# Kernel tuning notes

Hardware: AMD Instinct MI355X
Metric: run time of the kernel (lower is better)

Reference implementation:

```python
import jax, jax.numpy as jnp
import numpy as np

GRID_SIZE = 3
SPLINE_ORDER = 3
GRID_RANGE = (-1.0, 1.0)


def make_grid():
    # extended knot vector, shape (1, grid_size + 2*spline_order + 1) = (1, 10)
    h = (GRID_RANGE[1] - GRID_RANGE[0]) / GRID_SIZE
    pts = np.arange(-SPLINE_ORDER, GRID_SIZE + SPLINE_ORDER + 1, dtype=np.float32) * h + GRID_RANGE[0]
    return jnp.asarray(pts[None, :])  # broadcasts over in_features


def b_splines(x, grid):
    # x: (B, in) -> bases: (B, in, grid_size + spline_order)
    x = x[..., None]  # (B, in, 1)
    bases = ((x >= grid[:, :-1]) & (x < grid[:, 1:])).astype(x.dtype)
    for k in range(1, SPLINE_ORDER + 1):
        left = (x - grid[:, : -(k + 1)]) / (grid[:, k:-1] - grid[:, : -(k + 1)])
        right = (grid[:, k + 1:] - x) / (grid[:, k + 1:] - grid[:, 1:-k])
        bases = left * bases[..., :-1] + right * bases[..., 1:]
    return bases


def kan_linear(x, base_w, spline_w, scaler, grid):
    # efficient-kan KANLinear: silu(x)@base_w.T + b_splines(x) contracted with scaled spline weights
    base_out = jnp.einsum('bi,oi->bo', jax.nn.silu(x), base_w)
    bases = b_splines(x, grid)  # (B, in, 6)
    spline_out = jnp.einsum('bik,oik->bo', bases, spline_w * scaler[..., None])
    return base_out + spline_out


def layer_norm(x, gamma, beta, eps=1e-5):
    mu = jnp.mean(x, axis=-1, keepdims=True)
    var = jnp.mean(jnp.square(x - mu), axis=-1, keepdims=True)
    return (x - mu) * jax.lax.rsqrt(var + eps) * gamma + beta


def setup_inputs() -> dict:
    key = jax.random.key(0)
    ks = jax.random.split(key, 8)
    B, D_IN, D_HID, D_OUT = 16384, 1280, 512, 229
    NB = GRID_SIZE + SPLINE_ORDER  # 6 basis functions per input feature
    s1 = 1.0 / np.sqrt(D_IN)
    s2 = 1.0 / np.sqrt(D_HID)
    return {
        'x': jax.random.normal(ks[0], (B, D_IN), dtype=jnp.float32),
        'base_w1': jax.random.normal(ks[1], (D_HID, D_IN), dtype=jnp.float32) * s1,
        'spline_w1': jax.random.normal(ks[2], (D_HID, D_IN, NB), dtype=jnp.float32) * s1,
        'scaler1': jax.random.normal(ks[3], (D_HID, D_IN), dtype=jnp.float32) * 0.1 + 1.0,
        'ln_gamma': jnp.ones((D_HID,), dtype=jnp.float32),
        'ln_beta': jnp.zeros((D_HID,), dtype=jnp.float32),
        'base_w2': jax.random.normal(ks[4], (D_OUT, D_HID), dtype=jnp.float32) * s2,
        'spline_w2': jax.random.normal(ks[5], (D_OUT, D_HID, NB), dtype=jnp.float32) * s2,
        'scaler2': jax.random.normal(ks[6], (D_OUT, D_HID), dtype=jnp.float32) * 0.1 + 1.0,
    }


def reference(x, base_w1, spline_w1, scaler1, ln_gamma, ln_beta, base_w2, spline_w2, scaler2):
    grid = make_grid()
    h = kan_linear(x, base_w1, spline_w1, scaler1, grid)   # (B, 512)
    h = layer_norm(h, ln_gamma, ln_beta)                    # dropout: identity at inference
    out = kan_linear(h, base_w2, spline_w2, scaler2, grid)  # (B, 229)
    return out
```

## Files before the change

### kernel.cpp

```cpp
#include <hip/hip_runtime.h>


typedef short s16x8 __attribute__((ext_vector_type(8)));
typedef float f32x4 __attribute__((ext_vector_type(4)));

__device__ __forceinline__ void dma16(const void* g, void* l) {
  __builtin_amdgcn_global_load_lds(
      (const __attribute__((address_space(1))) unsigned int*)g,
      (__attribute__((address_space(3))) unsigned int*)l, 16, 0, 0);
}

template <int N>
__device__ __forceinline__ void wait_vm() {
  if constexpr (N == 0)      asm volatile("s_waitcnt vmcnt(0)" ::: "memory");
  else if constexpr (N == 5) asm volatile("s_waitcnt vmcnt(5)" ::: "memory");
  else if constexpr (N == 9) asm volatile("s_waitcnt vmcnt(9)" ::: "memory");
  else static_assert(N == 0, "unsupported vmcnt");
}

__device__ __forceinline__ unsigned pk2(float lo, float hi) {
  unsigned a = __float_as_uint(lo), b = __float_as_uint(hi);
  a = a + 0x7fffu + ((a >> 16) & 1u);
  b = b + 0x7fffu + ((b >> 16) & 1u);
  return __builtin_amdgcn_perm(b, a, 0x07060302u);
}

__device__ __forceinline__ unsigned short f2bf(float f) {
  unsigned u = __float_as_uint(f);
  unsigned r = u + 0x7fffu + ((u >> 16) & 1u);
  return (unsigned short)(r >> 16);
}

__device__ __forceinline__ uint4 kan_act8(float x) {
  float e = __expf(-x);
  float s = x * __builtin_amdgcn_rcpf(1.0f + e);
  float u = fmaf(x, 1.5f, 4.5f);
  float d[10];
#pragma unroll
  for (int j = 0; j < 10; ++j) d[j] = u - (float)j;
  float b1[8];
#pragma unroll
  for (int j = 0; j < 8; ++j) b1[j] = fmaxf(0.0f, 1.0f - fabsf(d[j + 1]));
  float B2[7];
#pragma unroll
  for (int j = 0; j < 7; ++j) B2[j] = d[j] * b1[j] - d[j + 3] * b1[j + 1];
  float b3[6];
#pragma unroll
  for (int j = 0; j < 6; ++j)
    b3[j] = (d[j] * B2[j] - d[j + 4] * B2[j + 1]) * (1.0f / 6.0f);
  uint4 r;
  r.x = pk2(s, b3[0]);
  r.y = pk2(b3[1], b3[2]);
  r.z = pk2(b3[3], b3[4]);
  r.w = pk2(b3[5], 0.0f);
  return r;
}

__global__ __launch_bounds__(256) void prep_w(
    const float* __restrict__ base_w, const float* __restrict__ spline_w,
    const float* __restrict__ scaler, short* __restrict__ Wp,
    int F, int Nvalid) {
  int i = blockIdx.x * 256 + threadIdx.x;
  int n = blockIdx.y;
  if (i >= F) return;
  s16x8 v;
#pragma unroll
  for (int k = 0; k < 8; ++k) v[k] = 0;
  if (n < Nvalid) {
    int idx = n * F + i;
    float sc = scaler[idx];
    v[0] = (short)f2bf(base_w[idx]);
#pragma unroll
    for (int k = 0; k < 6; ++k) v[1 + k] = (short)f2bf(spline_w[idx * 6 + k] * sc);
  }
  int p = (i & ~3) | ((i & 3) ^ (n & 3));
  *(s16x8*)&Wp[((size_t)n * F + p) * 8] = v;
}

template <int BN>
__global__ __launch_bounds__(256, 4) void kan_gemm(
    const float* __restrict__ X, const short* __restrict__ W,
    float* __restrict__ Cp, int F, int span, long long pstride,
    int ldc, int ncols) {
  constexpr int NT = BN / 64;
  constexpr int IE = BN / 64;
  __shared__ __align__(16) short As[2][64 * 32];
  __shared__ __align__(16) short Bs[2][BN * 32];

  const int t    = threadIdx.x;
  const int lane = t & 63;
  const int w    = t >> 6;
  const int m0   = blockIdx.x * 64;
  const int c0   = blockIdx.y * BN;
  const int f0   = blockIdx.z * span;

  const int wcol = w * (BN / 4);
  const int mrow = lane & 15;
  const int q    = lane >> 4;
  const int qs   = (q ^ (mrow & 3)) * 8;

  const int a_lo = mrow * 32 + qs;
  const int b_lo = (wcol + mrow) * 32 + qs;

  const int sr = t >> 2, sj = t & 3;
  const float* xq = X + (size_t)(m0 + sr) * F + f0 + sj;
  const int aw = sr * 32 + ((sj ^ (sr & 3)) * 8);

  const int drow = c0 + wcol + (lane >> 2);
  const int dchk = lane & 3;
  const char* wg = (const char*)W + ((size_t)drow * F + f0 + dchk) * 16;
  const size_t gistr = (size_t)16 * F * 16;

  f32x4 acc[4][NT] = {};
  const int nsteps = span >> 2;

  float x0 = *xq;
#pragma unroll
  for (int e = 0; e < IE; ++e)
    dma16(wg + e * gistr, &Bs[0][(wcol + e * 16) * 32]);
  {
    uint4 av = kan_act8(x0);
    *(uint4*)&As[0][aw] = av;
  }
  float xA = (nsteps > 1) ? xq[4] : 0.0f;
  __syncthreads();

  for (int ks = 0; ks < nsteps; ++ks) {
    const int cb = ks & 1, nb = cb ^ 1;
    const bool more = (ks + 1 < nsteps);

    float xB = 0.0f;
    if (ks + 2 < nsteps) xB = xq[(size_t)(ks + 2) * 4];

    if (more) {
#pragma unroll
      for (int e = 0; e < IE; ++e)
        dma16(wg + (size_t)(ks + 1) * 64 + e * gistr,
              &Bs[nb][(wcol + e * 16) * 32]);
      wait_vm<IE + 1>();
    } else {
      wait_vm<0>();
    }

    const short* Ac = As[cb];
    const short* Bc = Bs[cb];
    s16x8 af[4], bfr[NT];
#pragma unroll
    for (int it = 0; it < 4; ++it)
      af[it] = *(const s16x8*)(Ac + a_lo + it * (16 * 32));
#pragma unroll
    for (int jt = 0; jt < NT; ++jt)
      bfr[jt] = *(const s16x8*)(Bc + b_lo + jt * (16 * 32));
#pragma unroll
    for (int b = 0; b < NT; ++b)
#pragma unroll
      for (int a = 0; a < 4; ++a)
        acc[a][b] = __builtin_amdgcn_mfma_f32_16x16x32_bf16(
            af[a], bfr[b], acc[a][b], 0, 0, 0);

    if (more) {
      uint4 av = kan_act8(xA);
      *(uint4*)&As[nb][aw] = av;
      xA = xB;
    }
    asm volatile("s_waitcnt lgkmcnt(0)" ::: "memory");
    __builtin_amdgcn_s_barrier();
  }

  float* cpt = Cp + (size_t)blockIdx.z * (size_t)pstride;
#pragma unroll
  for (int a = 0; a < 4; ++a) {
#pragma unroll
    for (int b = 0; b < NT; ++b) {
      int col = c0 + wcol + b * 16 + mrow;
      if (col < ncols) {
#pragma unroll
        for (int r = 0; r < 4; ++r) {
          int row = m0 + a * 16 + (lane >> 4) * 4 + r;
          cpt[(size_t)row * ldc + col] = acc[a][b][r];
        }
      }
    }
  }
}

__global__ __launch_bounds__(256) void ln_reduce(
    const float* __restrict__ p0, const float* __restrict__ p1,
    float* __restrict__ h, const float* __restrict__ gamma,
    const float* __restrict__ beta, int nparts) {
  int lane = threadIdx.x & 63;
  int wv   = threadIdx.x >> 6;
  int row  = blockIdx.x * 4 + wv;
  size_t base = (size_t)row * 512 + lane * 8;
  f32x4 v0 = *(const f32x4*)(p0 + base);
  f32x4 v1 = *(const f32x4*)(p0 + base + 4);
  if (nparts == 2) {
    f32x4 u0 = *(const f32x4*)(p1 + base);
    f32x4 u1 = *(const f32x4*)(p1 + base + 4);
#pragma unroll
    for (int k = 0; k < 4; ++k) { v0[k] += u0[k]; v1[k] += u1[k]; }
  }
  float s = 0.f, s2 = 0.f;
#pragma unroll
  for (int k = 0; k < 4; ++k) { s += v0[k] + v1[k]; s2 += v0[k]*v0[k] + v1[k]*v1[k]; }
#pragma unroll
  for (int m = 32; m >= 1; m >>= 1) {
    s  += __shfl_xor(s,  m, 64);
    s2 += __shfl_xor(s2, m, 64);
  }
  float mean = s * (1.0f / 512.0f);
  float var  = s2 * (1.0f / 512.0f) - mean * mean;
  float rstd = rsqrtf(var + 1e-5f);
  const f32x4 g0 = *(const f32x4*)(gamma + lane * 8);
  const f32x4 g1 = *(const f32x4*)(gamma + lane * 8 + 4);
  const f32x4 be0 = *(const f32x4*)(beta + lane * 8);
  const f32x4 be1 = *(const f32x4*)(beta + lane * 8 + 4);
#pragma unroll
  for (int k = 0; k < 4; ++k) {
    v0[k] = (v0[k] - mean) * rstd * g0[k] + be0[k];
    v1[k] = (v1[k] - mean) * rstd * g1[k] + be1[k];
  }
  *(f32x4*)(h + base) = v0;
  *(f32x4*)(h + base + 4) = v1;
}

__global__ __launch_bounds__(256) void out_reduce(
    const float* __restrict__ p0, const float* __restrict__ p1,
    float* __restrict__ out, int nparts) {
  int idx = blockIdx.x * 256 + threadIdx.x;
  int row = idx >> 8;
  int c   = idx & 255;
  float v = p0[idx];
  if (nparts == 2) v += p1[idx];
  if (c < 229) out[(size_t)row * 229 + c] = v;
}

extern "C" void kernel_launch(void* const* d_in, const int* in_sizes, int n_in,
                              void* d_out, int out_size, void* d_ws, size_t ws_size,
                              hipStream_t stream) {
  const float* x         = (const float*)d_in[0];
  const float* base_w1   = (const float*)d_in[1];
  const float* spline_w1 = (const float*)d_in[2];
  const float* scaler1   = (const float*)d_in[3];
  const float* ln_gamma  = (const float*)d_in[4];
  const float* ln_beta   = (const float*)d_in[5];
  const float* base_w2   = (const float*)d_in[6];
  const float* spline_w2 = (const float*)d_in[7];
  const float* scaler2   = (const float*)d_in[8];
  float* out = (float*)d_out;

  const int B = 16384, D_IN = 1280, D_HID = 512, D_OUT = 229;

  const size_t szW1 = (size_t)D_HID * D_IN * 8 * 2;
  const size_t szW2 = (size_t)256 * D_HID * 8 * 2;
  const size_t szH  = (size_t)B * D_HID * 4;
  const size_t szP  = (size_t)B * 512 * 4;
  char* ws = (char*)d_ws;
  short* W1p = (short*)ws;
  short* W2p = (short*)(ws + szW1);
  float* h   = (float*)(ws + szW1 + szW2);
  float* p0  = (float*)(ws + szW1 + szW2 + szH);
  float* p1  = (float*)(ws + szW1 + szW2 + szH + szP);

  const int parts = (ws_size >= szW1 + szW2 + szH + 2 * szP) ? 2 : 1;
  const long long pstride = (long long)(szP / 4);

  prep_w<<<dim3(D_IN / 256, D_HID), 256, 0, stream>>>(
      base_w1, spline_w1, scaler1, W1p, D_IN, D_HID);
  prep_w<<<dim3(D_HID / 256, 256), 256, 0, stream>>>(
      base_w2, spline_w2, scaler2, W2p, D_HID, D_OUT);

  kan_gemm<256><<<dim3(B / 64, D_HID / 256, parts), 256, 0, stream>>>(
      x, W1p, p0, D_IN, D_IN / parts, pstride, D_HID, D_HID);

  ln_reduce<<<dim3(B / 4), 256, 0, stream>>>(p0, p1, h, ln_gamma, ln_beta, parts);

  kan_gemm<256><<<dim3(B / 64, 1, parts), 256, 0, stream>>>(
      h, W2p, p0, D_HID, D_HID / parts, pstride, 256, 256);

  out_reduce<<<dim3(B * 256 / 256), 256, 0, stream>>>(p0, p1, out, parts);
}
```

Baseline: 466.8 us.

## Use 32x32 MFMA tiles and one 512-wide block for first KAN GEMM

Result: faster. 456.6 us (-2.2%).

```diff
diff --git a/kernel.cpp b/kernel.cpp
--- a/kernel.cpp
+++ b/kernel.cpp
@@ -3,6 +3,7 @@
 
 typedef short s16x8 __attribute__((ext_vector_type(8)));
 typedef float f32x4 __attribute__((ext_vector_type(4)));
+typedef float f32x16 __attribute__((ext_vector_type(16)));
 
 __device__ __forceinline__ void dma16(const void* g, void* l) {
   __builtin_amdgcn_global_load_lds(
@@ -13,8 +14,8 @@
 template <int N>
 __device__ __forceinline__ void wait_vm() {
   if constexpr (N == 0)      asm volatile("s_waitcnt vmcnt(0)" ::: "memory");
+  else if constexpr (N == 4) asm volatile("s_waitcnt vmcnt(4)" ::: "memory");
   else if constexpr (N == 5) asm volatile("s_waitcnt vmcnt(5)" ::: "memory");
-  else if constexpr (N == 9) asm volatile("s_waitcnt vmcnt(9)" ::: "memory");
   else static_assert(N == 0, "unsupported vmcnt");
 }
 
@@ -73,17 +74,15 @@
 #pragma unroll
     for (int k = 0; k < 6; ++k) v[1 + k] = (short)f2bf(spline_w[idx * 6 + k] * sc);
   }
-  int p = (i & ~3) | ((i & 3) ^ (n & 3));
+  int p = (i & ~3) | ((i & 3) ^ ((n >> 1) & 3));
   *(s16x8*)&Wp[((size_t)n * F + p) * 8] = v;
 }
 
 template <int BN>
-__global__ __launch_bounds__(256, 4) void kan_gemm(
+__global__ __launch_bounds__(BN, 4) void kan_gemm(
     const float* __restrict__ X, const short* __restrict__ W,
     float* __restrict__ Cp, int F, int span, long long pstride,
     int ldc, int ncols) {
-  constexpr int NT = BN / 64;
-  constexpr int IE = BN / 64;
   __shared__ __align__(16) short As[2][64 * 32];
   __shared__ __align__(16) short Bs[2][BN * 32];
 
@@ -91,38 +90,40 @@
   const int lane = t & 63;
   const int w    = t >> 6;
   const int m0   = blockIdx.x * 64;
-  const int c0   = blockIdx.y * BN;
   const int f0   = blockIdx.z * span;
 
-  const int wcol = w * (BN / 4);
-  const int mrow = lane & 15;
-  const int q    = lane >> 4;
-  const int qs   = (q ^ (mrow & 3)) * 8;
-
-  const int a_lo = mrow * 32 + qs;
-  const int b_lo = (wcol + mrow) * 32 + qs;
+  const int wcol = w * 64;
+  const int r5   = lane & 31;
+  const int hi   = lane >> 5;
+  const int e2   = (lane >> 1) & 3;
+
+  const int a_base = r5 * 32;
+  const int b_base = (wcol + r5) * 32;
+  const int koff0  = ((0 + hi) ^ e2) * 8;
+  const int koff1  = ((2 + hi) ^ e2) * 8;
 
   const int sr = t >> 2, sj = t & 3;
   const float* xq = X + (size_t)(m0 + sr) * F + f0 + sj;
-  const int aw = sr * 32 + ((sj ^ (sr & 3)) * 8);
-
-  const int drow = c0 + wcol + (lane >> 2);
+  const int aw = sr * 32 + ((sj ^ ((sr >> 1) & 3)) * 8);
+  const bool actor = (t < 256);
+
+  const int drow = wcol + (lane >> 2);
   const int dchk = lane & 3;
   const char* wg = (const char*)W + ((size_t)drow * F + f0 + dchk) * 16;
   const size_t gistr = (size_t)16 * F * 16;
 
-  f32x4 acc[4][NT] = {};
+  f32x16 acc[2][2] = {};
   const int nsteps = span >> 2;
 
-  float x0 = *xq;
-#pragma unroll
-  for (int e = 0; e < IE; ++e)
+  float x0 = actor ? *xq : 0.0f;
+#pragma unroll
+  for (int e = 0; e < 4; ++e)
     dma16(wg + e * gistr, &Bs[0][(wcol + e * 16) * 32]);
-  {
+  if (actor) {
     uint4 av = kan_act8(x0);
     *(uint4*)&As[0][aw] = av;
   }
-  float xA = (nsteps > 1) ? xq[4] : 0.0f;
+  float xA = (actor && nsteps > 1) ? xq[4] : 0.0f;
   __syncthreads();
 
   for (int ks = 0; ks < nsteps; ++ks) {
@@ -130,35 +131,39 @@
     const bool more = (ks + 1 < nsteps);
 
     float xB = 0.0f;
-    if (ks + 2 < nsteps) xB = xq[(size_t)(ks + 2) * 4];
+    if (actor) {
+      int pf = ks + 2 < nsteps ? ks + 2 : nsteps - 1;
+      xB = xq[(size_t)pf * 4];
+    }
 
     if (more) {
 #pragma unroll
-      for (int e = 0; e < IE; ++e)
+      for (int e = 0; e < 4; ++e)
         dma16(wg + (size_t)(ks + 1) * 64 + e * gistr,
               &Bs[nb][(wcol + e * 16) * 32]);
-      wait_vm<IE + 1>();
+      if (actor) wait_vm<5>(); else wait_vm<4>();
     } else {
       wait_vm<0>();
     }
 
     const short* Ac = As[cb];
     const short* Bc = Bs[cb];
-    s16x8 af[4], bfr[NT];
-#pragma unroll
-    for (int it = 0; it < 4; ++it)
-      af[it] = *(const s16x8*)(Ac + a_lo + it * (16 * 32));
-#pragma unroll
-    for (int jt = 0; jt < NT; ++jt)
-      bfr[jt] = *(const s16x8*)(Bc + b_lo + jt * (16 * 32));
-#pragma unroll
-    for (int b = 0; b < NT; ++b)
-#pragma unroll
-      for (int a = 0; a < 4; ++a)
-        acc[a][b] = __builtin_amdgcn_mfma_f32_16x16x32_bf16(
-            af[a], bfr[b], acc[a][b], 0, 0, 0);
-
-    if (more) {
+#pragma unroll
+    for (int kk = 0; kk < 2; ++kk) {
+      const int ko = kk ? koff1 : koff0;
+      s16x8 af0 = *(const s16x8*)(Ac + a_base + ko);
+      s16x8 af1 = *(const s16x8*)(Ac + a_base + 1024 + ko);
+      s16x8 bf0 = *(const s16x8*)(Bc + b_base + ko);
+      s16x8 bf1 = *(const s16x8*)(Bc + b_base + 1024 + ko);
+      __builtin_amdgcn_s_setprio(1);
+      acc[0][0] = __builtin_amdgcn_mfma_f32_32x32x16_bf16(af0, bf0, acc[0][0], 0, 0, 0);
+      acc[0][1] = __builtin_amdgcn_mfma_f32_32x32x16_bf16(af0, bf1, acc[0][1], 0, 0, 0);
+      acc[1][0] = __builtin_amdgcn_mfma_f32_32x32x16_bf16(af1, bf0, acc[1][0], 0, 0, 0);
+      acc[1][1] = __builtin_amdgcn_mfma_f32_32x32x16_bf16(af1, bf1, acc[1][1], 0, 0, 0);
+      __builtin_amdgcn_s_setprio(0);
+    }
+
+    if (more && actor) {
       uint4 av = kan_act8(xA);
       *(uint4*)&As[nb][aw] = av;
       xA = xB;
@@ -169,15 +174,15 @@
 
   float* cpt = Cp + (size_t)blockIdx.z * (size_t)pstride;
 #pragma unroll
-  for (int a = 0; a < 4; ++a) {
-#pragma unroll
-    for (int b = 0; b < NT; ++b) {
-      int col = c0 + wcol + b * 16 + mrow;
+  for (int mt = 0; mt < 2; ++mt) {
+#pragma unroll
+    for (int nt = 0; nt < 2; ++nt) {
+      int col = wcol + nt * 32 + r5;
       if (col < ncols) {
 #pragma unroll
-        for (int r = 0; r < 4; ++r) {
-          int row = m0 + a * 16 + (lane >> 4) * 4 + r;
-          cpt[(size_t)row * ldc + col] = acc[a][b][r];
+        for (int reg = 0; reg < 16; ++reg) {
+          int row = m0 + mt * 32 + (reg & 3) + 8 * (reg >> 2) + 4 * hi;
+          cpt[(size_t)row * ldc + col] = acc[mt][nt][reg];
         }
       }
     }
@@ -270,7 +275,7 @@
   prep_w<<<dim3(D_HID / 256, 256), 256, 0, stream>>>(
       base_w2, spline_w2, scaler2, W2p, D_HID, D_OUT);
 
-  kan_gemm<256><<<dim3(B / 64, D_HID / 256, parts), 256, 0, stream>>>(
+  kan_gemm<512><<<dim3(B / 64, 1, parts), 512, 0, stream>>>(
       x, W1p, p0, D_IN, D_IN / parts, pstride, D_HID, D_HID);
 
   ln_reduce<<<dim3(B / 4), 256, 0, stream>>>(p0, p1, h, ln_gamma, ln_beta, parts);
```
